# Optimization experiments

Hardware: AMD Instinct MI355X
Metric: run time of the kernel (lower is better)

Reference implementation:

```python
import jax, jax.numpy as jnp
import numpy as np

DIM = 768
HEADS = 12
SCALE = DIM ** (-0.5)  # NOTE: original scales by full dim, not per-head dim


def setup_inputs() -> dict:
    key = jax.random.key(0)
    k1, k2, k3 = jax.random.split(key, 3)
    b, n = 4, 2048
    x = jax.random.normal(k1, (b, n, DIM), dtype=jnp.float32)
    # torch Linear layout: weight [out_features, in_features]
    w_qkv = jax.random.normal(k2, (3 * DIM, DIM), dtype=jnp.float32) * (DIM ** -0.5)
    b_qkv = jnp.zeros((3 * DIM,), dtype=jnp.float32)
    w_out = jax.random.normal(k3, (DIM, DIM), dtype=jnp.float32) * (DIM ** -0.5)
    b_out = jnp.zeros((DIM,), dtype=jnp.float32)
    return {"x": x, "w_qkv": w_qkv, "b_qkv": b_qkv, "w_out": w_out, "b_out": b_out}


def reference(x, w_qkv, b_qkv, w_out, b_out):
    b, n, dim = x.shape
    h = HEADS
    d = dim // h
    qkv = x @ w_qkv.T + b_qkv                       # [b, n, 3*dim]
    # rearrange 'b n (qkv h d) -> qkv b h n d'
    qkv = qkv.reshape(b, n, 3, h, d).transpose(2, 0, 3, 1, 4)
    q, k, v = qkv[0], qkv[1], qkv[2]                # each [b, h, n, d]
    dots = jnp.einsum('bhid,bhjd->bhij', q, k) * SCALE
    attn = jax.nn.softmax(dots, axis=-1)
    out = jnp.einsum('bhij,bhjd->bhid', attn, v)    # [b, h, n, d]
    out = out.transpose(0, 2, 1, 3).reshape(b, n, h * d)
    out = out @ w_out.T + b_out
    return out
```

## Files before the change

### kernel.cpp

```cpp
#include <hip/hip_runtime.h>
#include <hip/hip_bf16.h>
#include <stdint.h>
#include <math.h>

#define HEADS 12
#define HD 64
#define NB 4
#define NSEQ 2048
#define DIM 768
#define MROWS (NB*NSEQ)
#define QKV_OUT (3*DIM)
#define QSCALE (0.03608439182435161f * 1.4426950408889634f)

typedef __bf16 bf16;
typedef __attribute__((ext_vector_type(8))) __bf16 bf16x8;
typedef __attribute__((ext_vector_type(4))) __bf16 bf16x4;
typedef __attribute__((ext_vector_type(4))) float f32x4;
typedef __attribute__((ext_vector_type(16))) float f32x16;
typedef unsigned int uint;

typedef __attribute__((address_space(1))) void gvoid_t;
typedef __attribute__((address_space(3))) void lvoid_t;
#define GLOAD_LDS16(src, dst) \
  __builtin_amdgcn_global_load_lds((gvoid_t*)(src), (lvoid_t*)(dst), 16, 0, 0)

__device__ __forceinline__ float fast_exp2(float x) {
  float r; asm("v_exp_f32 %0, %1" : "=v"(r) : "v"(x)); return r;
}
__device__ __forceinline__ uint cvtpk_bf16(float a, float b) {
  uint r; asm("v_cvt_pk_bf16_f32 %0, %1, %2" : "=v"(r) : "v"(a), "v"(b)); return r;
}
__device__ __forceinline__ void plswap(uint &a, uint &b) {
  asm("v_permlane32_swap_b32 %0, %1" : "+v"(a), "+v"(b));
}

__global__ void k_cvt3(const float* __restrict__ x, const float* __restrict__ wqkv,
                       const float* __restrict__ wout,
                       bf16* __restrict__ xb, bf16* __restrict__ wqkvb,
                       bf16* __restrict__ woutb) {
  const int n0 = MROWS * DIM / 4, n1 = QKV_OUT * DIM / 4, n2 = DIM * DIM / 4;
  int i = blockIdx.x * blockDim.x + threadIdx.x;
  const float* src; bf16* dst;
  if (i < n0)           { src = x;    dst = xb; }
  else if (i < n0 + n1) { src = wqkv; dst = wqkvb; i -= n0; }
  else if (i < n0 + n1 + n2) { src = wout; dst = woutb; i -= n0 + n1; }
  else return;
  const f32x4 v = ((const f32x4*)src)[i];
  bf16x4 o;
#pragma unroll
  for (int j = 0; j < 4; ++j) o[j] = (bf16)v[j];
  ((bf16x4*)dst)[i] = o;
}

template<int ROWBYTES>
__device__ __forceinline__ void stage_swz(const bf16* g, int grow0, int gstride,
                                          int gcol0, char* ldsbuf) {
  constexpr int CPR = ROWBYTES / 16;
  const int t = threadIdx.x;
  const int wid = t >> 6;
#pragma unroll
  for (int call = 0; call < 2; ++call) {
    const int o = call * 4096 + t * 16;
    const int r = o / ROWBYTES;
    const int c = (o % ROWBYTES) / 16;
    const int cs = c ^ (r & (CPR - 1));
    const bf16* src = g + (long)(grow0 + r) * gstride + gcol0 + cs * 8;
    char* dst = ldsbuf + call * 4096 + wid * 1024;
    GLOAD_LDS16(src, dst);
  }
}

template<int ROWBYTES>
__device__ __forceinline__ bf16x8 frag_ld(const char* buf, int row, int chunk) {
  constexpr int CPR = ROWBYTES / 16;
  const int cs = chunk ^ (row & (CPR - 1));
  return *(const bf16x8*)(buf + row * ROWBYTES + cs * 16);
}

__device__ __forceinline__ void build_pfrags(const f32x16 &p, bf16x8 *f) {
  union { uint u[4]; bf16x8 v; } A, B;
  uint a0 = cvtpk_bf16(p[0], p[1]),  b0 = cvtpk_bf16(p[4], p[5]);   plswap(a0, b0);
  uint a1 = cvtpk_bf16(p[2], p[3]),  b1 = cvtpk_bf16(p[6], p[7]);   plswap(a1, b1);
  A.u[0] = a0; A.u[1] = a1; A.u[2] = b0; A.u[3] = b1;
  uint a2 = cvtpk_bf16(p[8], p[9]),  b2 = cvtpk_bf16(p[12], p[13]); plswap(a2, b2);
  uint a3 = cvtpk_bf16(p[10], p[11]), b3 = cvtpk_bf16(p[14], p[15]); plswap(a3, b3);
  B.u[0] = a2; B.u[1] = a3; B.u[2] = b2; B.u[3] = b3;
  f[0] = A.v; f[1] = B.v;
}

__device__ __forceinline__ void gemm_core(const bf16* __restrict__ A, const bf16* __restrict__ Bm,
                                          int m0, int n0, f32x16 acc[2][2], char* lds) {
  const int t = threadIdx.x;
  const int lane = t & 63, wid = t >> 6;
  const int l31 = lane & 31, hi = lane >> 5;
  const int wm = wid >> 1, wn = wid & 1;
#pragma unroll
  for (int i = 0; i < 2; ++i)
#pragma unroll
    for (int j = 0; j < 2; ++j)
#pragma unroll
      for (int r = 0; r < 16; ++r) acc[i][j][r] = 0.f;

  stage_swz<64>(A, m0, DIM, 0, lds);
  stage_swz<64>(Bm, n0, DIM, 0, lds + 16384);
  __syncthreads();
  int cur = 0;
  const int NT = DIM / 32;
  for (int kt = 0; kt < NT; ++kt) {
    char* Acur = lds + cur * 8192;
    char* Bcur = lds + 16384 + cur * 8192;
    if (kt + 1 < NT) {
      stage_swz<64>(A, m0, DIM, (kt + 1) * 32, lds + (cur ^ 1) * 8192);
      stage_swz<64>(Bm, n0, DIM, (kt + 1) * 32, lds + 16384 + (cur ^ 1) * 8192);
    }
    bf16x8 af[2][2], bfr[2][2];
#pragma unroll
    for (int i = 0; i < 2; ++i)
#pragma unroll
      for (int h = 0; h < 2; ++h) {
        af[i][h]  = frag_ld<64>(Acur, wm * 64 + i * 32 + l31, h * 2 + hi);
        bfr[i][h] = frag_ld<64>(Bcur, wn * 64 + i * 32 + l31, h * 2 + hi);
      }
#pragma unroll
    for (int h = 0; h < 2; ++h)
#pragma unroll
      for (int i = 0; i < 2; ++i)
#pragma unroll
        for (int j = 0; j < 2; ++j)
          acc[i][j] = __builtin_amdgcn_mfma_f32_32x32x16_bf16(af[i][h], bfr[j][h], acc[i][j], 0, 0, 0);
    __syncthreads();
    cur ^= 1;
  }
}

__global__ void __launch_bounds__(256) k_qkv_gemm(const bf16* __restrict__ xb,
                                                  const bf16* __restrict__ wb,
                                                  const float* __restrict__ bqkv,
                                                  bf16* __restrict__ qb,
                                                  bf16* __restrict__ kb,
                                                  bf16* __restrict__ vtb) {
  __shared__ alignas(128) char lds[32768];
  const int m0 = blockIdx.x * 128;
  const int n0 = blockIdx.y * 128;
  const int region = n0 / DIM;
  const int t = threadIdx.x;
  const int lane = t & 63, wid = t >> 6;
  const int l31 = lane & 31, hi = lane >> 5;
  const int wm = wid >> 1, wn = wid & 1;
  f32x16 acc[2][2];

  if (region < 2) {
    gemm_core(wb, xb, n0, m0, acc, lds);
    bf16* dst0 = (region == 0) ? qb : kb;
#pragma unroll
    for (int i = 0; i < 2; ++i)
#pragma unroll
      for (int q = 0; q < 4; ++q) {
        const int o = n0 + wm * 64 + i * 32 + 8 * q + 4 * hi;
        const f32x4 b4 = *(const f32x4*)(bqkv + o);
        const int oc = o - region * DIM;
        const int h = oc >> 6, d = oc & 63;
#pragma unroll
        for (int j = 0; j < 2; ++j) {
          const int mb = m0 + wn * 64 + j * 32 + l31;
          const int bb = mb >> 11, nn = mb & 2047;
          bf16x4 pk;
#pragma unroll
          for (int s = 0; s < 4; ++s) {
            float v = acc[i][j][4 * q + s] + b4[s];
            if (region == 0) v *= QSCALE;
            pk[s] = (bf16)v;
          }
          *(bf16x4*)(dst0 + ((long)((bb * HEADS + h) * NSEQ + nn)) * HD + d) = pk;
        }
      }
  } else {
    gemm_core(xb, wb, m0, n0, acc, lds);
#pragma unroll
    for (int j = 0; j < 2; ++j) {
      const int o = n0 + wn * 64 + j * 32 + l31;
      const float bias = bqkv[o];
      const int oc = o - 2 * DIM;
      const int h = oc >> 6, d = oc & 63;
#pragma unroll
      for (int i = 0; i < 2; ++i)
#pragma unroll
        for (int q = 0; q < 4; ++q) {
          const int rowb = m0 + wm * 64 + i * 32 + 8 * q + 4 * hi;
          const int bb = rowb >> 11, nn = rowb & 2047;
          bf16x4 pk;
#pragma unroll
          for (int s = 0; s < 4; ++s) pk[s] = (bf16)(acc[i][j][4 * q + s] + bias);
          *(bf16x4*)(vtb + ((long)((bb * HEADS + h) * HD + d)) * NSEQ + nn) = pk;
        }
    }
  }
}

__global__ void __launch_bounds__(256, 2) k_attn(const bf16* __restrict__ qb,
                                                 const bf16* __restrict__ kb,
                                                 const bf16* __restrict__ vtb,
                                                 bf16* __restrict__ ob) {
  __shared__ alignas(128) char lds[65536];
  char* ldsc = lds;
  const int bh = blockIdx.x;
  const int qt = blockIdx.y;
  const int t = threadIdx.x;
  const int lane = t & 63, wid = t >> 6;
  const int l31 = lane & 31, hi = lane >> 5;
  const bf16* qg = qb + (long)bh * NSEQ * HD;
  const bf16* kg = kb + (long)bh * NSEQ * HD;
  const bf16* vg = vtb + (long)bh * HD * NSEQ;
  const int q0w = qt * 128 + wid * 32;

  bf16x8 bq[4];
#pragma unroll
  for (int ks = 0; ks < 4; ++ks)
    bq[ks] = *(const bf16x8*)(qg + (long)(q0w + l31) * HD + ks * 16 + hi * 8);

  const int rbase_k = l31 * 128 + ((hi ^ (l31 & 7)) << 4);
  const int rbase_v = l31 * 256 + ((hi ^ (l31 & 15)) << 4);

  const int cs_k = (t & 7) ^ ((t >> 3) & 7);
  const bf16* kbase = kg + (t >> 3) * 64 + cs_k * 8;
  const int cs_v = (t & 15) ^ ((t >> 4) & 15);
  const bf16* vbase = vg + (long)(t >> 4) * NSEQ + cs_v * 8;
  const int dofs = wid << 10;

  auto stage_k = [&](int j, int slot) {
#pragma unroll
    for (int c = 0; c < 4; ++c)
      GLOAD_LDS16(kbase + j * 8192 + c * 2048, ldsc + slot * 16384 + c * 4096 + dofs);
  };
  auto stage_v = [&](int j, int slot) {
#pragma unroll
    for (int c = 0; c < 4; ++c)
      GLOAD_LDS16(vbase + (long)j * 128 + (long)c * 32768,
                  ldsc + 32768 + slot * 16384 + c * 4096 + dofs);
  };

  f32x16 ot0, ot1;
#pragma unroll
  for (int r = 0; r < 16; ++r) { ot0[r] = 0.f; ot1[r] = 0.f; }
  float l_run = 0.f;
  bf16x8 pf[8];

  auto qkt128 = [&](int kslot, f32x16 S[4]) {
#pragma unroll
    for (int sub = 0; sub < 4; ++sub)
#pragma unroll
      for (int r = 0; r < 16; ++r) S[sub][r] = 0.f;
    __builtin_amdgcn_s_setprio(1);
#pragma unroll
    for (int ks = 0; ks < 4; ++ks) {
      const int a = kslot * 16384 + (rbase_k ^ (ks << 5));
#pragma unroll
      for (int sub = 0; sub < 4; ++sub) {
        const bf16x8 ak = *(const bf16x8*)(ldsc + a + sub * 4096);
        S[sub] = __builtin_amdgcn_mfma_f32_32x32x16_bf16(ak, bq[ks], S[sub], 0, 0, 0);
      }
    }
    __builtin_amdgcn_s_setprio(0);
  };

  auto exppack128 = [&](f32x16 S[4]) {
    float rs = 0.f;
#pragma unroll
    for (int sub = 0; sub < 4; ++sub) {
      float a = 0.f;
#pragma unroll
      for (int r = 0; r < 16; ++r) { S[sub][r] = fast_exp2(S[sub][r]); a += S[sub][r]; }
      rs += a;
      build_pfrags(S[sub], &pf[2 * sub]);
    }
    l_run += rs;
  };

  auto pv128 = [&](int vslot) {
    __builtin_amdgcn_s_setprio(1);
#pragma unroll
    for (int s = 0; s < 8; ++s) {
      const int a = 32768 + vslot * 16384 + (rbase_v ^ (s << 5));
      const bf16x8 av0 = *(const bf16x8*)(ldsc + a);
      ot0 = __builtin_amdgcn_mfma_f32_32x32x16_bf16(av0, pf[s], ot0, 0, 0, 0);
      const bf16x8 av1 = *(const bf16x8*)(ldsc + a + 8192);
      ot1 = __builtin_amdgcn_mfma_f32_32x32x16_bf16(av1, pf[s], ot1, 0, 0, 0);
    }
    __builtin_amdgcn_s_setprio(0);
  };

  stage_k(0, 0);
  asm volatile("s_waitcnt vmcnt(0)" ::: "memory");
  __builtin_amdgcn_s_barrier();
  asm volatile("" ::: "memory");
  {
    f32x16 S[4];
    qkt128(0, S);
    stage_k(1, 1);
    stage_v(0, 0);
    exppack128(S);
  }

  for (int tt = 0; tt < 15; ++tt) {
    asm volatile("s_waitcnt vmcnt(0)" ::: "memory");
    __builtin_amdgcn_s_barrier();
    asm volatile("" ::: "memory");
    stage_k(tt + 2 < 16 ? tt + 2 : 15, tt & 1);
    stage_v(tt + 1, (tt + 1) & 1);
    f32x16 S[4];
    if (wid & 1) {
      qkt128((tt + 1) & 1, S);
      pv128(tt & 1);
    } else {
      pv128(tt & 1);
      qkt128((tt + 1) & 1, S);
    }
    exppack128(S);
  }
  asm volatile("s_waitcnt vmcnt(0)" ::: "memory");
  __builtin_amdgcn_s_barrier();
  asm volatile("" ::: "memory");
  pv128(1);

  l_run += __shfl_xor(l_run, 32);
  const float inv = 1.f / l_run;
#pragma unroll
  for (int r = 0; r < 16; ++r) { ot0[r] *= inv; ot1[r] *= inv; }
  __builtin_amdgcn_s_barrier();
  char* tw = lds + wid * 4352;
#pragma unroll
  for (int g = 0; g < 4; ++g) {
    uint2 w0, w1;
    w0.x = cvtpk_bf16(ot0[4 * g], ot0[4 * g + 1]);
    w0.y = cvtpk_bf16(ot0[4 * g + 2], ot0[4 * g + 3]);
    w1.x = cvtpk_bf16(ot1[4 * g], ot1[4 * g + 1]);
    w1.y = cvtpk_bf16(ot1[4 * g + 2], ot1[4 * g + 3]);
    const int d0 = 8 * g + 4 * hi;
    *(uint2*)(tw + l31 * 136 + d0 * 2) = w0;
    *(uint2*)(tw + l31 * 136 + (32 + d0) * 2) = w1;
  }
  const int b_ = bh / HEADS, h_ = bh - b_ * HEADS;
#pragma unroll
  for (int pass = 0; pass < 4; ++pass) {
    const int row = pass * 8 + (lane >> 3);
    const bf16x8 vv = *(const bf16x8*)(tw + row * 136 + (lane & 7) * 16);
    *(bf16x8*)(ob + ((long)(b_ * NSEQ + q0w + row)) * DIM + h_ * 64 + (lane & 7) * 8) = vv;
  }
}

__global__ void __launch_bounds__(256) k_out_gemm(const bf16* __restrict__ ab,
                                                  const bf16* __restrict__ wob,
                                                  const float* __restrict__ bout,
                                                  float* __restrict__ out) {
  __shared__ alignas(128) char lds[32768];
  const int m0 = blockIdx.x * 128;
  const int n0 = blockIdx.y * 128;
  f32x16 acc[2][2];
  gemm_core(wob, ab, n0, m0, acc, lds);

  const int t = threadIdx.x;
  const int lane = t & 63, wid = t >> 6;
  const int l31 = lane & 31, hi = lane >> 5;
  const int wm = wid >> 1, wn = wid & 1;
#pragma unroll
  for (int i = 0; i < 2; ++i)
#pragma unroll
    for (int q = 0; q < 4; ++q) {
      const int o = n0 + wm * 64 + i * 32 + 8 * q + 4 * hi;
      const f32x4 b4 = *(const f32x4*)(bout + o);
#pragma unroll
      for (int j = 0; j < 2; ++j) {
        const int mb = m0 + wn * 64 + j * 32 + l31;
        f32x4 v;
#pragma unroll
        for (int s = 0; s < 4; ++s) v[s] = acc[i][j][4 * q + s] + b4[s];
        *(f32x4*)(out + (long)mb * DIM + o) = v;
      }
    }
}

extern "C" void kernel_launch(void* const* d_in, const int* in_sizes, int n_in,
                              void* d_out, int out_size, void* d_ws, size_t ws_size,
                              hipStream_t stream) {
  const float* x    = (const float*)d_in[0];
  const float* wqkv = (const float*)d_in[1];
  const float* bqkv = (const float*)d_in[2];
  const float* wout = (const float*)d_in[3];
  const float* bout = (const float*)d_in[4];
  float* out = (float*)d_out;
  char* ws = (char*)d_ws;

  bf16* xb    = (bf16*)(ws);
  bf16* wqkvb = (bf16*)(ws + 12582912);
  bf16* woutb = (bf16*)(ws + 16121856);
  bf16* qb    = (bf16*)(ws + 17301504);
  bf16* kb    = (bf16*)(ws + 29884416);
  bf16* vtb   = (bf16*)(ws + 42467328);
  bf16* ab    = (bf16*)(ws + 55050240);

  const int ncvt4 = MROWS * DIM / 4 + QKV_OUT * DIM / 4 + DIM * DIM / 4;
  k_cvt3<<<(ncvt4 + 255) / 256, 256, 0, stream>>>(x, wqkv, wout, xb, wqkvb, woutb);

  k_qkv_gemm<<<dim3(MROWS / 128, QKV_OUT / 128), 256, 0, stream>>>(xb, wqkvb, bqkv, qb, kb, vtb);
  k_attn<<<dim3(NB * HEADS, NSEQ / 128), 256, 0, stream>>>(qb, kb, vtb, ab);
  k_out_gemm<<<dim3(MROWS / 128, DIM / 128), 256, 0, stream>>>(ab, woutb, bout, out);
}
```

Before: 144.4 us.

## Restructure attention to two waves with 64 query rows each and 64-key tiles

The attention kernel now runs 128-thread blocks, two waves each covering 64 query rows, in place of four waves covering 32 rows each. Every K/V fragment read from LDS now feeds two MFMAs, cutting LDS read traffic per MFMA in half. KV tiles shrink from 128 to 64 keys, with 32 loop iterations instead of 16, and K moves to a triple-buffered ring. Total LDS drops to 40 KB, so more blocks can fit per CU. In exchange, each wave holds twice as many accumulator registers and there are more barriers per block.

Measured after the change: 152.4 us. 5.5% more time.

```diff
diff --git a/kernel.cpp b/kernel.cpp
--- a/kernel.cpp
+++ b/kernel.cpp
@@ -197,11 +197,11 @@
   }
 }
 
-__global__ void __launch_bounds__(256, 2) k_attn(const bf16* __restrict__ qb,
+__global__ void __launch_bounds__(128, 2) k_attn(const bf16* __restrict__ qb,
                                                  const bf16* __restrict__ kb,
                                                  const bf16* __restrict__ vtb,
                                                  bf16* __restrict__ ob) {
-  __shared__ alignas(128) char lds[65536];
+  __shared__ alignas(128) char lds[40960];
   char* ldsc = lds;
   const int bh = blockIdx.x;
   const int qt = blockIdx.y;
@@ -211,82 +211,87 @@
   const bf16* qg = qb + (long)bh * NSEQ * HD;
   const bf16* kg = kb + (long)bh * NSEQ * HD;
   const bf16* vg = vtb + (long)bh * HD * NSEQ;
-  const int q0w = qt * 128 + wid * 32;
-
-  bf16x8 bq[4];
+  const int q0w = qt * 128 + wid * 64;
+
+  bf16x8 bq[4][2];
 #pragma unroll
   for (int ks = 0; ks < 4; ++ks)
-    bq[ks] = *(const bf16x8*)(qg + (long)(q0w + l31) * HD + ks * 16 + hi * 8);
-
-  const int rbase_k = l31 * 128 + ((hi ^ (l31 & 7)) << 4);
-  const int rbase_v = l31 * 256 + ((hi ^ (l31 & 15)) << 4);
-
-  const int cs_k = (t & 7) ^ ((t >> 3) & 7);
-  const bf16* kbase = kg + (t >> 3) * 64 + cs_k * 8;
-  const int cs_v = (t & 15) ^ ((t >> 4) & 15);
-  const bf16* vbase = vg + (long)(t >> 4) * NSEQ + cs_v * 8;
+#pragma unroll
+    for (int h = 0; h < 2; ++h)
+      bq[ks][h] = *(const bf16x8*)(qg + (long)(q0w + h * 32 + l31) * HD + ks * 16 + hi * 8);
+
+  const int rbase = l31 * 128 + (((hi ^ l31) & 7) << 4);
+
+  const int cs = (t & 7) ^ ((t >> 3) & 7);
+  const bf16* kbase = kg + (t >> 3) * 64 + cs * 8;
+  const bf16* vbase = vg + (long)(t >> 3) * NSEQ + cs * 8;
   const int dofs = wid << 10;
 
   auto stage_k = [&](int j, int slot) {
 #pragma unroll
     for (int c = 0; c < 4; ++c)
-      GLOAD_LDS16(kbase + j * 8192 + c * 2048, ldsc + slot * 16384 + c * 4096 + dofs);
+      GLOAD_LDS16(kbase + j * 4096 + c * 1024, ldsc + slot * 8192 + c * 2048 + dofs);
   };
   auto stage_v = [&](int j, int slot) {
 #pragma unroll
     for (int c = 0; c < 4; ++c)
-      GLOAD_LDS16(vbase + (long)j * 128 + (long)c * 32768,
-                  ldsc + 32768 + slot * 16384 + c * 4096 + dofs);
+      GLOAD_LDS16(vbase + (long)j * 64 + (long)c * 32768,
+                  ldsc + 24576 + slot * 8192 + c * 2048 + dofs);
   };
 
-  f32x16 ot0, ot1;
-#pragma unroll
-  for (int r = 0; r < 16; ++r) { ot0[r] = 0.f; ot1[r] = 0.f; }
-  float l_run = 0.f;
-  bf16x8 pf[8];
-
-  auto qkt128 = [&](int kslot, f32x16 S[4]) {
-#pragma unroll
-    for (int sub = 0; sub < 4; ++sub)
-#pragma unroll
-      for (int r = 0; r < 16; ++r) S[sub][r] = 0.f;
+  f32x16 ot00, ot01, ot10, ot11;
+#pragma unroll
+  for (int r = 0; r < 16; ++r) { ot00[r] = 0.f; ot01[r] = 0.f; ot10[r] = 0.f; ot11[r] = 0.f; }
+  float l0 = 0.f, l1 = 0.f;
+  bf16x8 pf0[4], pf1[4];
+
+  auto qkt = [&](int kslot, f32x16 &S00, f32x16 &S01, f32x16 &S10, f32x16 &S11) {
+#pragma unroll
+    for (int r = 0; r < 16; ++r) { S00[r] = 0.f; S01[r] = 0.f; S10[r] = 0.f; S11[r] = 0.f; }
     __builtin_amdgcn_s_setprio(1);
 #pragma unroll
     for (int ks = 0; ks < 4; ++ks) {
-      const int a = kslot * 16384 + (rbase_k ^ (ks << 5));
-#pragma unroll
-      for (int sub = 0; sub < 4; ++sub) {
-        const bf16x8 ak = *(const bf16x8*)(ldsc + a + sub * 4096);
-        S[sub] = __builtin_amdgcn_mfma_f32_32x32x16_bf16(ak, bq[ks], S[sub], 0, 0, 0);
-      }
+      const int a = (rbase ^ (ks << 5)) + kslot * 8192;
+      const bf16x8 ak0 = *(const bf16x8*)(ldsc + a);
+      const bf16x8 ak1 = *(const bf16x8*)(ldsc + a + 4096);
+      S00 = __builtin_amdgcn_mfma_f32_32x32x16_bf16(ak0, bq[ks][0], S00, 0, 0, 0);
+      S10 = __builtin_amdgcn_mfma_f32_32x32x16_bf16(ak0, bq[ks][1], S10, 0, 0, 0);
+      S01 = __builtin_amdgcn_mfma_f32_32x32x16_bf16(ak1, bq[ks][0], S01, 0, 0, 0);
+      S11 = __builtin_amdgcn_mfma_f32_32x32x16_bf16(ak1, bq[ks][1], S11, 0, 0, 0);
     }
     __builtin_amdgcn_s_setprio(0);
   };
 
-  auto exppack128 = [&](f32x16 S[4]) {
-    float rs = 0.f;
-#pragma unroll
-    for (int sub = 0; sub < 4; ++sub) {
-      float a = 0.f;
-#pragma unroll
-      for (int r = 0; r < 16; ++r) { S[sub][r] = fast_exp2(S[sub][r]); a += S[sub][r]; }
-      rs += a;
-      build_pfrags(S[sub], &pf[2 * sub]);
-    }
-    l_run += rs;
+  auto pv = [&](int vslot) {
+    __builtin_amdgcn_s_setprio(1);
+#pragma unroll
+    for (int s = 0; s < 4; ++s) {
+      const int a = (rbase ^ (s << 5)) + 24576 + vslot * 8192;
+      const bf16x8 av0 = *(const bf16x8*)(ldsc + a);
+      const bf16x8 av1 = *(const bf16x8*)(ldsc + a + 4096);
+      ot00 = __builtin_amdgcn_mfma_f32_32x32x16_bf16(av0, pf0[s], ot00, 0, 0, 0);
+      ot10 = __builtin_amdgcn_mfma_f32_32x32x16_bf16(av0, pf1[s], ot10, 0, 0, 0);
+      ot01 = __builtin_amdgcn_mfma_f32_32x32x16_bf16(av1, pf0[s], ot01, 0, 0, 0);
+      ot11 = __builtin_amdgcn_mfma_f32_32x32x16_bf16(av1, pf1[s], ot11, 0, 0, 0);
+    }
+    __builtin_amdgcn_s_setprio(0);
   };
 
-  auto pv128 = [&](int vslot) {
-    __builtin_amdgcn_s_setprio(1);
-#pragma unroll
-    for (int s = 0; s < 8; ++s) {
-      const int a = 32768 + vslot * 16384 + (rbase_v ^ (s << 5));
-      const bf16x8 av0 = *(const bf16x8*)(ldsc + a);
-      ot0 = __builtin_amdgcn_mfma_f32_32x32x16_bf16(av0, pf[s], ot0, 0, 0, 0);
-      const bf16x8 av1 = *(const bf16x8*)(ldsc + a + 8192);
-      ot1 = __builtin_amdgcn_mfma_f32_32x32x16_bf16(av1, pf[s], ot1, 0, 0, 0);
-    }
-    __builtin_amdgcn_s_setprio(0);
+  auto exppack = [&](f32x16 &S00, f32x16 &S01, f32x16 &S10, f32x16 &S11) {
+    float a0 = 0.f, a1 = 0.f, b0 = 0.f, b1 = 0.f;
+#pragma unroll
+    for (int r = 0; r < 16; ++r) {
+      S00[r] = fast_exp2(S00[r]); a0 += S00[r];
+      S01[r] = fast_exp2(S01[r]); a1 += S01[r];
+      S10[r] = fast_exp2(S10[r]); b0 += S10[r];
+      S11[r] = fast_exp2(S11[r]); b1 += S11[r];
+    }
+    l0 += a0 + a1;
+    l1 += b0 + b1;
+    build_pfrags(S00, &pf0[0]);
+    build_pfrags(S01, &pf0[2]);
+    build_pfrags(S10, &pf1[0]);
+    build_pfrags(S11, &pf1[2]);
   };
 
   stage_k(0, 0);
@@ -294,54 +299,61 @@
   __builtin_amdgcn_s_barrier();
   asm volatile("" ::: "memory");
   {
-    f32x16 S[4];
-    qkt128(0, S);
+    f32x16 S00, S01, S10, S11;
+    qkt(0, S00, S01, S10, S11);
     stage_k(1, 1);
     stage_v(0, 0);
-    exppack128(S);
-  }
-
-  for (int tt = 0; tt < 15; ++tt) {
+    exppack(S00, S01, S10, S11);
+  }
+
+  for (int tt = 0; tt < 31; ++tt) {
     asm volatile("s_waitcnt vmcnt(0)" ::: "memory");
     __builtin_amdgcn_s_barrier();
     asm volatile("" ::: "memory");
-    stage_k(tt + 2 < 16 ? tt + 2 : 15, tt & 1);
+    stage_k(tt + 2 < 32 ? tt + 2 : 31, (tt + 2) % 3);
     stage_v(tt + 1, (tt + 1) & 1);
-    f32x16 S[4];
+    f32x16 S00, S01, S10, S11;
     if (wid & 1) {
-      qkt128((tt + 1) & 1, S);
-      pv128(tt & 1);
+      qkt((tt + 1) % 3, S00, S01, S10, S11);
+      pv(tt & 1);
     } else {
-      pv128(tt & 1);
-      qkt128((tt + 1) & 1, S);
-    }
-    exppack128(S);
+      pv(tt & 1);
+      qkt((tt + 1) % 3, S00, S01, S10, S11);
+    }
+    exppack(S00, S01, S10, S11);
   }
   asm volatile("s_waitcnt vmcnt(0)" ::: "memory");
   __builtin_amdgcn_s_barrier();
   asm volatile("" ::: "memory");
-  pv128(1);
-
-  l_run += __shfl_xor(l_run, 32);
-  const float inv = 1.f / l_run;
-#pragma unroll
-  for (int r = 0; r < 16; ++r) { ot0[r] *= inv; ot1[r] *= inv; }
-  __builtin_amdgcn_s_barrier();
-  char* tw = lds + wid * 4352;
+  pv(1);
+
+  l0 += __shfl_xor(l0, 32);
+  l1 += __shfl_xor(l1, 32);
+  const float i0 = 1.f / l0, i1 = 1.f / l1;
+#pragma unroll
+  for (int r = 0; r < 16; ++r) { ot00[r] *= i0; ot01[r] *= i0; ot10[r] *= i1; ot11[r] *= i1; }
+  char* tw = lds + wid * 8704;
 #pragma unroll
   for (int g = 0; g < 4; ++g) {
+    const int d0 = 8 * g + 4 * hi;
     uint2 w0, w1;
-    w0.x = cvtpk_bf16(ot0[4 * g], ot0[4 * g + 1]);
-    w0.y = cvtpk_bf16(ot0[4 * g + 2], ot0[4 * g + 3]);
-    w1.x = cvtpk_bf16(ot1[4 * g], ot1[4 * g + 1]);
-    w1.y = cvtpk_bf16(ot1[4 * g + 2], ot1[4 * g + 3]);
-    const int d0 = 8 * g + 4 * hi;
+    w0.x = cvtpk_bf16(ot00[4 * g], ot00[4 * g + 1]);
+    w0.y = cvtpk_bf16(ot00[4 * g + 2], ot00[4 * g + 3]);
+    w1.x = cvtpk_bf16(ot01[4 * g], ot01[4 * g + 1]);
+    w1.y = cvtpk_bf16(ot01[4 * g + 2], ot01[4 * g + 3]);
     *(uint2*)(tw + l31 * 136 + d0 * 2) = w0;
     *(uint2*)(tw + l31 * 136 + (32 + d0) * 2) = w1;
+    uint2 x0, x1;
+    x0.x = cvtpk_bf16(ot10[4 * g], ot10[4 * g + 1]);
+    x0.y = cvtpk_bf16(ot10[4 * g + 2], ot10[4 * g + 3]);
+    x1.x = cvtpk_bf16(ot11[4 * g], ot11[4 * g + 1]);
+    x1.y = cvtpk_bf16(ot11[4 * g + 2], ot11[4 * g + 3]);
+    *(uint2*)(tw + (32 + l31) * 136 + d0 * 2) = x0;
+    *(uint2*)(tw + (32 + l31) * 136 + (32 + d0) * 2) = x1;
   }
   const int b_ = bh / HEADS, h_ = bh - b_ * HEADS;
 #pragma unroll
-  for (int pass = 0; pass < 4; ++pass) {
+  for (int pass = 0; pass < 8; ++pass) {
     const int row = pass * 8 + (lane >> 3);
     const bf16x8 vv = *(const bf16x8*)(tw + row * 136 + (lane & 7) * 16);
     *(bf16x8*)(ob + ((long)(b_ * NSEQ + q0w + row)) * DIM + h_ * 64 + (lane & 7) * 8) = vv;
@@ -402,6 +414,6 @@
   k_cvt3<<<(ncvt4 + 255) / 256, 256, 0, stream>>>(x, wqkv, wout, xb, wqkvb, woutb);
 
   k_qkv_gemm<<<dim3(MROWS / 128, QKV_OUT / 128), 256, 0, stream>>>(xb, wqkvb, bqkv, qb, kb, vtb);
-  k_attn<<<dim3(NB * HEADS, NSEQ / 128), 256, 0, stream>>>(qb, kb, vtb, ab);
+  k_attn<<<dim3(NB * HEADS, NSEQ / 128), 128, 0, stream>>>(qb, kb, vtb, ab);
   k_out_gemm<<<dim3(MROWS / 128, DIM / 128), 256, 0, stream>>>(ab, woutb, bout, out);
 }
```
